# Optimization experiments

Hardware: AMD Instinct MI355X
Metric: run time of the kernel (lower is better)

The kernel has to match this reference:

```python
import jax, jax.numpy as jnp
import numpy as np

NUM_ITERATIONS = 3


def _squash(t, axis=-1):
    sq = jnp.sum(t * t, axis=axis, keepdims=True)
    # scale * t / sqrt(sq), matching torch: sq/(1+sq) * t / sqrt(sq)
    return (sq / (1.0 + sq)) * t / jnp.sqrt(sq)


def setup_inputs() -> dict:
    key = jax.random.key(0)
    k1, k2, k3 = jax.random.split(key, 3)
    B, R, CI = 64, 1152, 64
    C, O = 32, 32
    x = jax.random.normal(k1, (B, R, CI), dtype=jnp.float32)
    cond = jax.random.normal(k2, (B, CI), dtype=jnp.float32)
    route_weights = jax.random.normal(k3, (C, R, CI, O), dtype=jnp.float32)
    return {"x": x, "cond": cond, "route_weights": route_weights}


def reference(x, cond, route_weights):
    # priors: [C, B, R, O] (original keeps an extra singleton dim 3; dropped here,
    # logits broadcast over the out dim identically so math is unchanged)
    priors = jnp.einsum('bri,crio->cbro', x, route_weights)
    logits = jnp.zeros(priors.shape[:3] + (1,), dtype=priors.dtype)
    outputs = None
    for idx in range(NUM_ITERATIONS):
        probs = jax.nn.softmax(logits, axis=2)          # softmax over route dim
        outputs = _squash(jnp.sum(probs * priors, axis=2, keepdims=True))  # [C,B,1,O]
        if idx != NUM_ITERATIONS - 1:
            # agreement update: [C,B,R,1]
            logits = logits + jnp.sum(priors * outputs, axis=-1, keepdims=True)
    out = jnp.squeeze(outputs, axis=2)                  # [C,B,O]
    return jnp.transpose(out, (1, 0, 2))                # [B,C,O]
```

## Files before the change

kernel.cpp:

```cpp
#include <hip/hip_runtime.h>
#include <stdint.h>

#define NB 64
#define NR 1152
#define NI 64
#define NC 32
#define NO 32

typedef __attribute__((ext_vector_type(8))) short bf16x8;
typedef __attribute__((ext_vector_type(4))) float f32x4;
typedef float float4v __attribute__((ext_vector_type(4)));

__device__ __forceinline__ uint16_t f2bf(float f) {
  uint32_t u = __float_as_uint(f);
  return (uint16_t)((u + 0x7FFFu + ((u >> 16) & 1u)) >> 16);
}
__device__ __forceinline__ float bf2f(uint16_t h) {
  return __uint_as_float(((uint32_t)h) << 16);
}

__global__ __launch_bounds__(256, 4)
void k_xcvt(const float* __restrict__ x, uint16_t* __restrict__ xh,
            uint16_t* __restrict__ xl) {
  const int r = blockIdx.x;
  const int t = threadIdx.x;
  const int b = t >> 2, i0 = (t & 3) * 16;
  const float* src = x + ((size_t)b * NR + r) * NI + i0;

  union { uint16_t us[16]; uint4 v[2]; } hb, lb;
#pragma unroll
  for (int k = 0; k < 4; ++k) {
    const float4v v = __builtin_nontemporal_load(
        reinterpret_cast<const float4v*>(src + 4 * k));
#pragma unroll
    for (int j = 0; j < 4; ++j) {
      const uint16_t h = f2bf(v[j]);
      hb.us[k * 4 + j] = h;
      lb.us[k * 4 + j] = f2bf(v[j] - bf2f(h));
    }
  }
  const size_t dst = ((size_t)r * NB + b) * NI + i0;
  *reinterpret_cast<uint4*>(xh + dst)     = hb.v[0];
  *reinterpret_cast<uint4*>(xh + dst + 8) = hb.v[1];
  *reinterpret_cast<uint4*>(xl + dst)     = lb.v[0];
  *reinterpret_cast<uint4*>(xl + dst + 8) = lb.v[1];
}

__global__ __launch_bounds__(256, 6)
void k_priors(const uint16_t* __restrict__ xh, const uint16_t* __restrict__ xl,
              const float* __restrict__ W, float* __restrict__ P) {
  __shared__ __align__(16) uint16_t xhs[NB * NI];
  __shared__ __align__(16) uint16_t xls[NB * NI];
  __shared__ __align__(16) uint16_t whs[NO * NI];
  __shared__ __align__(16) uint16_t wls[NO * NI];

  const int tid  = threadIdx.x;
  const int lane = tid & 63;
  const int mt   = tid >> 6;
  const int c    = blockIdx.x;
  const int r    = blockIdx.y;

  {
    const int b = tid >> 2, i0 = (tid & 3) * 16;
    const size_t src = ((size_t)r * NB + b) * NI + i0;
    const int sw = (b & 7) << 4;
    const int a0 = (b * 128 + i0 * 2) ^ sw;
    const int a1 = (b * 128 + (i0 + 8) * 2) ^ sw;
    uint4 v;
    v = *reinterpret_cast<const uint4*>(xh + src);
    *reinterpret_cast<uint4*>((char*)xhs + a0) = v;
    v = *reinterpret_cast<const uint4*>(xh + src + 8);
    *reinterpret_cast<uint4*>((char*)xhs + a1) = v;
    v = *reinterpret_cast<const uint4*>(xl + src);
    *reinterpret_cast<uint4*>((char*)xls + a0) = v;
    v = *reinterpret_cast<const uint4*>(xl + src + 8);
    *reinterpret_cast<uint4*>((char*)xls + a1) = v;
  }
  {
    const int i2 = tid >> 3, o0 = (tid & 7) * 4;
    const float* wsrc = W + (((size_t)c * NR + r) * NI + 2 * i2) * NO + o0;
    const float4v f0 = __builtin_nontemporal_load(
        reinterpret_cast<const float4v*>(wsrc));
    const float4v f1 = __builtin_nontemporal_load(
        reinterpret_cast<const float4v*>(wsrc + NO));
#pragma unroll
    for (int j = 0; j < 4; ++j) {
      const int o = o0 + j;
      const float fa = f0[j], fb = f1[j];
      const uint16_t ha = f2bf(fa), hb = f2bf(fb);
      const uint16_t la = f2bf(fa - bf2f(ha)), lb = f2bf(fb - bf2f(hb));
      const int ad = (o * 128 + i2 * 4) ^ ((o & 7) << 4);
      *reinterpret_cast<uint32_t*>((char*)whs + ad) = (uint32_t)ha | ((uint32_t)hb << 16);
      *reinterpret_cast<uint32_t*>((char*)wls + ad) = (uint32_t)la | ((uint32_t)lb << 16);
    }
  }
  __syncthreads();

  const int lm = lane & 15;
  const int lg = lane >> 4;
  const int brow = mt * 16 + lm;
  const int aswz = (brow & 7) << 4;
  const int a0 = (brow * 128 + (8 * lg) * 2) ^ aswz;
  const int a1 = (brow * 128 + (32 + 8 * lg) * 2) ^ aswz;
  const int or0 = lm, or1 = 16 + lm;
  const int b00 = (or0 * 128 + (8 * lg) * 2) ^ ((or0 & 7) << 4);
  const int b01 = (or0 * 128 + (32 + 8 * lg) * 2) ^ ((or0 & 7) << 4);
  const int b10 = (or1 * 128 + (8 * lg) * 2) ^ ((or1 & 7) << 4);
  const int b11 = (or1 * 128 + (32 + 8 * lg) * 2) ^ ((or1 & 7) << 4);

#define RD(arr, off) (*reinterpret_cast<const bf16x8*>((const char*)(arr) + (off)))
#define MFMA(A, B, C) __builtin_amdgcn_mfma_f32_16x16x32_bf16(A, B, C, 0, 0, 0)

  f32x4 acc0 = {0.f, 0.f, 0.f, 0.f}, acc1 = acc0;
  {
    bf16x8 a, b;
    a = RD(xhs, a0);
    b = RD(whs, b00); acc0 = MFMA(a, b, acc0);
    b = RD(whs, b10); acc1 = MFMA(a, b, acc1);
    b = RD(wls, b00); acc0 = MFMA(a, b, acc0);
    b = RD(wls, b10); acc1 = MFMA(a, b, acc1);
    a = RD(xhs, a1);
    b = RD(whs, b01); acc0 = MFMA(a, b, acc0);
    b = RD(whs, b11); acc1 = MFMA(a, b, acc1);
    b = RD(wls, b01); acc0 = MFMA(a, b, acc0);
    b = RD(wls, b11); acc1 = MFMA(a, b, acc1);
    a = RD(xls, a0);
    b = RD(whs, b00); acc0 = MFMA(a, b, acc0);
    b = RD(whs, b10); acc1 = MFMA(a, b, acc1);
    a = RD(xls, a1);
    b = RD(whs, b01); acc0 = MFMA(a, b, acc0);
    b = RD(whs, b11); acc1 = MFMA(a, b, acc1);
  }
#undef RD
#undef MFMA

#pragma unroll
  for (int reg = 0; reg < 4; ++reg) {
    const int b = mt * 16 + lg * 4 + reg;
    float* dst = P + (((size_t)c * NB + b) * NR + r) * NO;
    __builtin_nontemporal_store(acc0[reg], dst + lm);
    __builtin_nontemporal_store(acc1[reg], dst + 16 + lm);
  }
}

__device__ __forceinline__ void merge4(float& m, float& Z, float4& T,
                                       float m2, float Z2, const float4& T2) {
  const float mn = fmaxf(m, m2);
  const float a1 = __expf(m - mn), a2 = __expf(m2 - mn);
  Z   = Z * a1 + Z2 * a2;
  T.x = T.x * a1 + T2.x * a2;
  T.y = T.y * a1 + T2.y * a2;
  T.z = T.z * a1 + T2.z * a2;
  T.w = T.w * a1 + T2.w * a2;
  m = mn;
}

__global__ __launch_bounds__(1024, 1)
void k_route(const float* __restrict__ P, float* __restrict__ out) {
  __shared__ float red_s[16][8][8];
  __shared__ float u_s[NO];

  const int tid  = threadIdx.x;
  const int lane = tid & 63;
  const int wave = tid >> 6;
  const int sl   = tid & 7;
  const int grp  = tid >> 3;
  const int b    = blockIdx.x;
  const int c    = blockIdx.y;
  const float* Pb = P + ((size_t)c * NB + b) * ((size_t)NR * NO);

  float4 p[9];
#pragma unroll
  for (int j = 0; j < 9; ++j) {
    const float4v t = __builtin_nontemporal_load(
        reinterpret_cast<const float4v*>(Pb + (size_t)(grp + 128 * j) * NO + sl * 4));
    p[j].x = t.x; p[j].y = t.y; p[j].z = t.z; p[j].w = t.w;
  }

  {
    float4 T = p[0];
#pragma unroll
    for (int j = 1; j < 9; ++j) {
      T.x += p[j].x; T.y += p[j].y; T.z += p[j].z; T.w += p[j].w;
    }
#pragma unroll
    for (int off = 8; off <= 32; off <<= 1) {
      T.x += __shfl_xor(T.x, off); T.y += __shfl_xor(T.y, off);
      T.z += __shfl_xor(T.z, off); T.w += __shfl_xor(T.w, off);
    }
    if (lane < 8) {
      red_s[wave][sl][2] = T.x; red_s[wave][sl][3] = T.y;
      red_s[wave][sl][4] = T.z; red_s[wave][sl][5] = T.w;
    }
  }
  __syncthreads();
  if (tid < 8) {
    float4 S = make_float4(0.f, 0.f, 0.f, 0.f);
#pragma unroll
    for (int ww = 0; ww < 16; ++ww) {
      S.x += red_s[ww][tid][2]; S.y += red_s[ww][tid][3];
      S.z += red_s[ww][tid][4]; S.w += red_s[ww][tid][5];
    }
    S.x *= (1.f / NR); S.y *= (1.f / NR); S.z *= (1.f / NR); S.w *= (1.f / NR);
    float n2 = S.x * S.x + S.y * S.y + S.z * S.z + S.w * S.w;
    n2 += __shfl_xor(n2, 1); n2 += __shfl_xor(n2, 2); n2 += __shfl_xor(n2, 4);
    const float scale = n2 / ((1.f + n2) * sqrtf(n2));
    u_s[tid * 4 + 0] = S.x * scale; u_s[tid * 4 + 1] = S.y * scale;
    u_s[tid * 4 + 2] = S.z * scale; u_s[tid * 4 + 3] = S.w * scale;
  }
  __syncthreads();

  float4 u = *reinterpret_cast<const float4*>(&u_s[sl * 4]);
  float l1[9];

  for (int it = 1; it <= 2; ++it) {
    float m = -3.0e38f, Z = 0.f;
    float4 T = make_float4(0.f, 0.f, 0.f, 0.f);
#pragma unroll
    for (int j = 0; j < 9; ++j) {
      float d = p[j].x * u.x + p[j].y * u.y + p[j].z * u.z + p[j].w * u.w;
      d += __shfl_xor(d, 1); d += __shfl_xor(d, 2); d += __shfl_xor(d, 4);
      float l;
      if (it == 1) { l1[j] = d; l = d; }
      else         { l = l1[j] + d; }
      const float mn = fmaxf(m, l);
      const float a = __expf(m - mn);
      const float e = __expf(l - mn);
      Z   = Z * a + e;
      T.x = T.x * a + e * p[j].x; T.y = T.y * a + e * p[j].y;
      T.z = T.z * a + e * p[j].z; T.w = T.w * a + e * p[j].w;
      m = mn;
    }
#pragma unroll
    for (int off = 8; off <= 32; off <<= 1) {
      const float m2 = __shfl_xor(m, off);
      const float Z2 = __shfl_xor(Z, off);
      float4 T2;
      T2.x = __shfl_xor(T.x, off); T2.y = __shfl_xor(T.y, off);
      T2.z = __shfl_xor(T.z, off); T2.w = __shfl_xor(T.w, off);
      merge4(m, Z, T, m2, Z2, T2);
    }
    if (lane < 8) {
      red_s[wave][sl][0] = m;   red_s[wave][sl][1] = Z;
      red_s[wave][sl][2] = T.x; red_s[wave][sl][3] = T.y;
      red_s[wave][sl][4] = T.z; red_s[wave][sl][5] = T.w;
    }
    __syncthreads();
    if (tid < 8) {
      float mm = red_s[0][tid][0], ZZ = red_s[0][tid][1];
      float4 TT = make_float4(red_s[0][tid][2], red_s[0][tid][3],
                              red_s[0][tid][4], red_s[0][tid][5]);
#pragma unroll
      for (int ww = 1; ww < 16; ++ww) {
        const float4 T2 = make_float4(red_s[ww][tid][2], red_s[ww][tid][3],
                                      red_s[ww][tid][4], red_s[ww][tid][5]);
        merge4(mm, ZZ, TT, red_s[ww][tid][0], red_s[ww][tid][1], T2);
      }
      const float inv = 1.f / ZZ;
      float4 S = make_float4(TT.x * inv, TT.y * inv, TT.z * inv, TT.w * inv);
      float n2 = S.x * S.x + S.y * S.y + S.z * S.z + S.w * S.w;
      n2 += __shfl_xor(n2, 1); n2 += __shfl_xor(n2, 2); n2 += __shfl_xor(n2, 4);
      const float scale = n2 / ((1.f + n2) * sqrtf(n2));
      if (it == 1) {
        u_s[tid * 4 + 0] = S.x * scale; u_s[tid * 4 + 1] = S.y * scale;
        u_s[tid * 4 + 2] = S.z * scale; u_s[tid * 4 + 3] = S.w * scale;
      } else {
        *reinterpret_cast<float4*>(out + ((size_t)b * NC + c) * NO + tid * 4) =
            make_float4(S.x * scale, S.y * scale, S.z * scale, S.w * scale);
      }
    }
    __syncthreads();
    if (it == 1) u = *reinterpret_cast<const float4*>(&u_s[sl * 4]);
  }
}

extern "C" void kernel_launch(void* const* d_in, const int* in_sizes, int n_in,
                              void* d_out, int out_size, void* d_ws, size_t ws_size,
                              hipStream_t stream) {
  const float* x = (const float*)d_in[0];
  const float* W = (const float*)d_in[2];
  float* out = (float*)d_out;

  uint16_t* xh = (uint16_t*)d_ws;
  const size_t xbf_elems = (size_t)NR * NB * NI;
  uint16_t* xl = xh + xbf_elems;
  float* P = (float*)(xl + xbf_elems);

  k_xcvt<<<NR, 256, 0, stream>>>(x, xh, xl);
  k_priors<<<dim3(NC, NR), 256, 0, stream>>>(xh, xl, W, P);
  k_route<<<dim3(NB, NC), 1024, 0, stream>>>(P, out);
}
```

Baseline: 253.2 us.

## Process two classes per priors block and two batches per route block

```diff
diff --git a/kernel.cpp b/kernel.cpp
--- a/kernel.cpp
+++ b/kernel.cpp
@@ -46,18 +46,18 @@
   *reinterpret_cast<uint4*>(xl + dst + 8) = lb.v[1];
 }
 
-__global__ __launch_bounds__(256, 6)
+__global__ __launch_bounds__(256, 5)
 void k_priors(const uint16_t* __restrict__ xh, const uint16_t* __restrict__ xl,
               const float* __restrict__ W, float* __restrict__ P) {
   __shared__ __align__(16) uint16_t xhs[NB * NI];
   __shared__ __align__(16) uint16_t xls[NB * NI];
-  __shared__ __align__(16) uint16_t whs[NO * NI];
-  __shared__ __align__(16) uint16_t wls[NO * NI];
+  __shared__ __align__(16) uint16_t whs[2][NO * NI];
+  __shared__ __align__(16) uint16_t wls[2][NO * NI];
 
   const int tid  = threadIdx.x;
   const int lane = tid & 63;
   const int mt   = tid >> 6;
-  const int c    = blockIdx.x;
+  const int c0   = blockIdx.x * 2;
   const int r    = blockIdx.y;
 
   {
@@ -78,20 +78,25 @@
   }
   {
     const int i2 = tid >> 3, o0 = (tid & 7) * 4;
-    const float* wsrc = W + (((size_t)c * NR + r) * NI + 2 * i2) * NO + o0;
-    const float4v f0 = __builtin_nontemporal_load(
-        reinterpret_cast<const float4v*>(wsrc));
-    const float4v f1 = __builtin_nontemporal_load(
-        reinterpret_cast<const float4v*>(wsrc + NO));
-#pragma unroll
-    for (int j = 0; j < 4; ++j) {
-      const int o = o0 + j;
-      const float fa = f0[j], fb = f1[j];
-      const uint16_t ha = f2bf(fa), hb = f2bf(fb);
-      const uint16_t la = f2bf(fa - bf2f(ha)), lb = f2bf(fb - bf2f(hb));
-      const int ad = (o * 128 + i2 * 4) ^ ((o & 7) << 4);
-      *reinterpret_cast<uint32_t*>((char*)whs + ad) = (uint32_t)ha | ((uint32_t)hb << 16);
-      *reinterpret_cast<uint32_t*>((char*)wls + ad) = (uint32_t)la | ((uint32_t)lb << 16);
+#pragma unroll
+    for (int cc = 0; cc < 2; ++cc) {
+      const float* wsrc = W + (((size_t)(c0 + cc) * NR + r) * NI + 2 * i2) * NO + o0;
+      const float4v f0 = __builtin_nontemporal_load(
+          reinterpret_cast<const float4v*>(wsrc));
+      const float4v f1 = __builtin_nontemporal_load(
+          reinterpret_cast<const float4v*>(wsrc + NO));
+#pragma unroll
+      for (int j = 0; j < 4; ++j) {
+        const int o = o0 + j;
+        const float fa = f0[j], fb = f1[j];
+        const uint16_t ha = f2bf(fa), hbv = f2bf(fb);
+        const uint16_t la = f2bf(fa - bf2f(ha)), lbv = f2bf(fb - bf2f(hbv));
+        const int ad = (o * 128 + i2 * 4) ^ ((o & 7) << 4);
+        *reinterpret_cast<uint32_t*>((char*)whs[cc] + ad) =
+            (uint32_t)ha | ((uint32_t)hbv << 16);
+        *reinterpret_cast<uint32_t*>((char*)wls[cc] + ad) =
+            (uint32_t)la | ((uint32_t)lbv << 16);
+      }
     }
   }
   __syncthreads();
@@ -111,36 +116,40 @@
 #define RD(arr, off) (*reinterpret_cast<const bf16x8*>((const char*)(arr) + (off)))
 #define MFMA(A, B, C) __builtin_amdgcn_mfma_f32_16x16x32_bf16(A, B, C, 0, 0, 0)
 
-  f32x4 acc0 = {0.f, 0.f, 0.f, 0.f}, acc1 = acc0;
-  {
-    bf16x8 a, b;
-    a = RD(xhs, a0);
-    b = RD(whs, b00); acc0 = MFMA(a, b, acc0);
-    b = RD(whs, b10); acc1 = MFMA(a, b, acc1);
-    b = RD(wls, b00); acc0 = MFMA(a, b, acc0);
-    b = RD(wls, b10); acc1 = MFMA(a, b, acc1);
-    a = RD(xhs, a1);
-    b = RD(whs, b01); acc0 = MFMA(a, b, acc0);
-    b = RD(whs, b11); acc1 = MFMA(a, b, acc1);
-    b = RD(wls, b01); acc0 = MFMA(a, b, acc0);
-    b = RD(wls, b11); acc1 = MFMA(a, b, acc1);
-    a = RD(xls, a0);
-    b = RD(whs, b00); acc0 = MFMA(a, b, acc0);
-    b = RD(whs, b10); acc1 = MFMA(a, b, acc1);
-    a = RD(xls, a1);
-    b = RD(whs, b01); acc0 = MFMA(a, b, acc0);
-    b = RD(whs, b11); acc1 = MFMA(a, b, acc1);
+  const bf16x8 ah0 = RD(xhs, a0);
+  const bf16x8 ah1 = RD(xhs, a1);
+  const bf16x8 al0 = RD(xls, a0);
+  const bf16x8 al1 = RD(xls, a1);
+
+#pragma unroll
+  for (int cc = 0; cc < 2; ++cc) {
+    const uint16_t* wh = whs[cc];
+    const uint16_t* wl = wls[cc];
+    f32x4 acc0 = {0.f, 0.f, 0.f, 0.f}, acc1 = acc0;
+    bf16x8 b;
+    b = RD(wh, b00); acc0 = MFMA(ah0, b, acc0);
+    b = RD(wh, b10); acc1 = MFMA(ah0, b, acc1);
+    b = RD(wl, b00); acc0 = MFMA(ah0, b, acc0);
+    b = RD(wl, b10); acc1 = MFMA(ah0, b, acc1);
+    b = RD(wh, b01); acc0 = MFMA(ah1, b, acc0);
+    b = RD(wh, b11); acc1 = MFMA(ah1, b, acc1);
+    b = RD(wl, b01); acc0 = MFMA(ah1, b, acc0);
+    b = RD(wl, b11); acc1 = MFMA(ah1, b, acc1);
+    b = RD(wh, b00); acc0 = MFMA(al0, b, acc0);
+    b = RD(wh, b10); acc1 = MFMA(al0, b, acc1);
+    b = RD(wh, b01); acc0 = MFMA(al1, b, acc0);
+    b = RD(wh, b11); acc1 = MFMA(al1, b, acc1);
+
+#pragma unroll
+    for (int reg = 0; reg < 4; ++reg) {
+      const int bb = mt * 16 + lg * 4 + reg;
+      float* dst = P + (((size_t)(c0 + cc) * NB + bb) * NR + r) * NO;
+      __builtin_nontemporal_store(acc0[reg], dst + lm);
+      __builtin_nontemporal_store(acc1[reg], dst + 16 + lm);
+    }
   }
 #undef RD
 #undef MFMA
-
-#pragma unroll
-  for (int reg = 0; reg < 4; ++reg) {
-    const int b = mt * 16 + lg * 4 + reg;
-    float* dst = P + (((size_t)c * NB + b) * NR + r) * NO;
-    __builtin_nontemporal_store(acc0[reg], dst + lm);
-    __builtin_nontemporal_store(acc1[reg], dst + 16 + lm);
-  }
 }
 
 __device__ __forceinline__ void merge4(float& m, float& Z, float4& T,
@@ -155,28 +164,9 @@
   m = mn;
 }
 
-__global__ __launch_bounds__(1024, 1)
-void k_route(const float* __restrict__ P, float* __restrict__ out) {
-  __shared__ float red_s[16][8][8];
-  __shared__ float u_s[NO];
-
-  const int tid  = threadIdx.x;
-  const int lane = tid & 63;
-  const int wave = tid >> 6;
-  const int sl   = tid & 7;
-  const int grp  = tid >> 3;
-  const int b    = blockIdx.x;
-  const int c    = blockIdx.y;
-  const float* Pb = P + ((size_t)c * NB + b) * ((size_t)NR * NO);
-
-  float4 p[9];
-#pragma unroll
-  for (int j = 0; j < 9; ++j) {
-    const float4v t = __builtin_nontemporal_load(
-        reinterpret_cast<const float4v*>(Pb + (size_t)(grp + 128 * j) * NO + sl * 4));
-    p[j].x = t.x; p[j].y = t.y; p[j].z = t.z; p[j].w = t.w;
-  }
-
+__device__ __forceinline__ void route_body(
+    const float4 (&p)[9], int b, int c, int tid, int lane, int wave, int sl,
+    float (&red_s)[16][8][8], float (&u_s)[NO], float* __restrict__ out) {
   {
     float4 T = p[0];
 #pragma unroll
@@ -274,6 +264,39 @@
   }
 }
 
+__global__ __launch_bounds__(1024, 1)
+void k_route(const float* __restrict__ P, float* __restrict__ out) {
+  __shared__ float red_s[16][8][8];
+  __shared__ float u_s[NO];
+
+  const int tid  = threadIdx.x;
+  const int lane = tid & 63;
+  const int wave = tid >> 6;
+  const int sl   = tid & 7;
+  const int grp  = tid >> 3;
+  const int b0   = blockIdx.x * 2;
+  const int c    = blockIdx.y;
+  const float* Pb0 = P + ((size_t)c * NB + b0) * ((size_t)NR * NO);
+  const float* Pb1 = Pb0 + (size_t)NR * NO;
+
+  float4 pA[9], pB[9];
+#pragma unroll
+  for (int j = 0; j < 9; ++j) {
+    const float4v t = __builtin_nontemporal_load(
+        reinterpret_cast<const float4v*>(Pb0 + (size_t)(grp + 128 * j) * NO + sl * 4));
+    pA[j].x = t.x; pA[j].y = t.y; pA[j].z = t.z; pA[j].w = t.w;
+  }
+#pragma unroll
+  for (int j = 0; j < 9; ++j) {
+    const float4v t = __builtin_nontemporal_load(
+        reinterpret_cast<const float4v*>(Pb1 + (size_t)(grp + 128 * j) * NO + sl * 4));
+    pB[j].x = t.x; pB[j].y = t.y; pB[j].z = t.z; pB[j].w = t.w;
+  }
+
+  route_body(pA, b0,     c, tid, lane, wave, sl, red_s, u_s, out);
+  route_body(pB, b0 + 1, c, tid, lane, wave, sl, red_s, u_s, out);
+}
+
 extern "C" void kernel_launch(void* const* d_in, const int* in_sizes, int n_in,
                               void* d_out, int out_size, void* d_ws, size_t ws_size,
                               hipStream_t stream) {
@@ -287,6 +310,6 @@
   float* P = (float*)(xl + xbf_elems);
 
   k_xcvt<<<NR, 256, 0, stream>>>(x, xh, xl);
-  k_priors<<<dim3(NC, NR), 256, 0, stream>>>(xh, xl, W, P);
-  k_route<<<dim3(NB, NC), 1024, 0, stream>>>(P, out);
-}
+  k_priors<<<dim3(NC / 2, NR), 256, 0, stream>>>(xh, xl, W, P);
+  k_route<<<dim3(NB / 2, NC), 1024, 0, stream>>>(P, out);
+}
```

Result: slower. 307.8 us (+21.5%).
